# Kernel tuning notes

Measured on AMD Instinct MI355X. Metric: run time of the kernel, lower is better.

The kernel has to match this reference:

```python
import jax, jax.numpy as jnp
import numpy as np

SIGMA = 0.001
EPS_LOG = 1e-12
EPS_COS = 1e-8


def setup_inputs() -> dict:
    key = jax.random.key(0)
    k1, k2, k3, k4 = jax.random.split(key, 4)
    B, T, K, S, d = 32, 512, 8, 8, 300
    center_pos = jax.random.randint(k1, (B,), 0, T)
    query_token_ids = jax.random.randint(k2, (B, T), 0, 30000)
    center_sense_embeddings = jax.random.normal(k3, (B, K, d), dtype=jnp.float32)
    context_sense_embeddings = jax.random.normal(k4, (B, T - 1, S, d), dtype=jnp.float32)
    return {
        'center_pos': center_pos,
        'query_token_ids': query_token_ids,
        'center_sense_embeddings': center_sense_embeddings,
        'context_sense_embeddings': context_sense_embeddings,
    }


def reference(center_pos, query_token_ids, center_sense_embeddings, context_sense_embeddings):
    B, T = query_token_ids.shape
    d = center_sense_embeddings.shape[-1]
    # v: mean over senses of context tokens -> [B, C, d], C = T-1
    v = context_sense_embeddings.mean(axis=-2)
    # a: scaled dot between center senses and context vectors -> [B, C, K]
    a = jnp.einsum('bkd,bcd->bck', center_sense_embeddings, v) / jnp.sqrt(jnp.float32(d))
    # context positions: skip the center position (vectorized form of the per-batch loop)
    i = jnp.arange(T - 1)  # [C]
    ctx_pos = i[None, :] + (i[None, :] >= center_pos[:, None])  # [B, C]
    w = jnp.exp(-jnp.abs(ctx_pos - center_pos[:, None]).astype(jnp.float32) / SIGMA)
    logw = jnp.log(jnp.maximum(w, EPS_LOG))  # [B, C]
    alpha = jax.nn.softmax(a + logw[:, :, None], axis=1)  # softmax over context positions
    m = jnp.einsum('bck,bcd->bkd', alpha, v)  # [B, K, d]
    # cosine similarity along d (torch semantics: clamp each norm by eps)
    num = jnp.sum(center_sense_embeddings * m, axis=-1)
    n1 = jnp.linalg.norm(center_sense_embeddings, axis=-1)
    n2 = jnp.linalg.norm(m, axis=-1)
    s = num / (jnp.maximum(n1, EPS_COS) * jnp.maximum(n2, EPS_COS))  # [B, K]
    q = jax.nn.softmax(s, axis=-1)
    idx = jnp.argmax(q, axis=-1)  # [B]
    pooled = jnp.take_along_axis(center_sense_embeddings, idx[:, None, None], axis=1)[:, 0, :]  # [B, d]
    return pooled, q
```

## Files before the change

### kernel.cpp

```cpp
#include <hip/hip_runtime.h>

#define NB 32
#define NC 511
#define NK 8
#define NS 8
#define ND 300
#define ND4 75
#define NCH 16
#define CCHUNK 32
#define EPS_COS 1e-8f


typedef float nfloat4 __attribute__((ext_vector_type(4)));

__device__ __forceinline__ void n4add(nfloat4& a, const nfloat4& b) { a += b; }

__global__ __launch_bounds__(256) void k_va(const float* __restrict__ ctx,
                                            const float* __restrict__ cen,
                                            float* __restrict__ v,
                                            float* __restrict__ ea) {
    const int blk  = blockIdx.x >> 1;
    const int b    = blk >> 7;
    const int cgrp = blk & 127;
    const int w    = threadIdx.x >> 6;
    const int lane = threadIdx.x & 63;
    const int c = cgrp * 4 + w;
    if (c >= NC) return;

    const nfloat4* ctx4 = (const nfloat4*)ctx + (size_t)(b * NC + c) * NS * ND4;
    const int i0 = lane;
    const int i1 = lane + 64;
    const bool has1 = (i1 < ND4);

    nfloat4 X[NS];
#pragma unroll
    for (int s = 0; s < NS; ++s)
        X[s] = __builtin_nontemporal_load(&ctx4[s * ND4 + i0]);
    nfloat4 Y[NS] = {};
    if (has1) {
#pragma unroll
        for (int s = 0; s < NS; ++s)
            Y[s] = __builtin_nontemporal_load(&ctx4[s * ND4 + i1]);
    }

    n4add(X[0], X[1]); n4add(X[2], X[3]); n4add(X[4], X[5]); n4add(X[6], X[7]);
    n4add(X[0], X[2]); n4add(X[4], X[6]);
    n4add(X[0], X[4]);
    n4add(Y[0], Y[1]); n4add(Y[2], Y[3]); n4add(Y[4], Y[5]); n4add(Y[6], Y[7]);
    n4add(Y[0], Y[2]); n4add(Y[4], Y[6]);
    n4add(Y[0], Y[4]);
    const float inv = 0.125f;
    nfloat4 s0 = X[0] * inv;
    nfloat4 s1 = Y[0] * inv;

    nfloat4* v4 = (nfloat4*)v + (size_t)(b * NC + c) * ND4;
    v4[i0] = s0;
    if (has1) v4[i1] = s1;

    const nfloat4* cen4 = (const nfloat4*)cen + (size_t)b * NK * ND4;
    float pk[NK];
#pragma unroll
    for (int k = 0; k < NK; ++k) {
        nfloat4 ca = cen4[k * ND4 + i0];
        float p = ca.x * s0.x + ca.y * s0.y + ca.z * s0.z + ca.w * s0.w;
        if (has1) {
            nfloat4 cb = cen4[k * ND4 + i1];
            p += cb.x * s1.x + cb.y * s1.y + cb.z * s1.z + cb.w * s1.w;
        }
        pk[k] = p;
    }
#pragma unroll
    for (int off = 32; off; off >>= 1) {
#pragma unroll
        for (int k = 0; k < NK; ++k) pk[k] += __shfl_down(pk[k], off);
    }
    if (lane == 0) {
        const float scale = 0.057735026919f;
#pragma unroll
        for (int k = 0; k < NK; ++k)
            ea[(size_t)(b * NK + k) * NC + c] = __expf(pk[k] * scale);
    }
}

__global__ __launch_bounds__(320) void k_m(const float* __restrict__ v,
                                           const float* __restrict__ ea,
                                           float* __restrict__ part) {
    int b  = blockIdx.x >> 4;
    int ch = blockIdx.x & 15;
    int c0 = ch * CCHUNK;
    int cn = min(CCHUNK, NC - c0);
    __shared__ float al[NK][CCHUNK];
    int t = threadIdx.x;
    if (t < NK * CCHUNK) {
        int k = t >> 5, cc = t & 31;
        al[k][cc] = (cc < cn) ? ea[(size_t)(b * NK + k) * NC + c0 + cc] : 0.f;
    }
    __syncthreads();
    if (t < ND) {
        float acc[NK] = {0.f, 0.f, 0.f, 0.f, 0.f, 0.f, 0.f, 0.f};
        const float* vp = v + ((size_t)b * NC + c0) * ND + t;
        for (int cc = 0; cc < cn; ++cc) {
            float vv = vp[(size_t)cc * ND];
#pragma unroll
            for (int k = 0; k < NK; ++k) acc[k] += al[k][cc] * vv;
        }
        float* pp = part + ((size_t)(ch * NB + b) * NK) * ND + t;
#pragma unroll
        for (int k = 0; k < NK; ++k) pp[(size_t)k * ND] = acc[k];
    }
}

__global__ __launch_bounds__(256) void k_final(const float* __restrict__ part,
                                               const float* __restrict__ cen,
                                               float* __restrict__ out) {
    int b = blockIdx.x;
    __shared__ float m[NK * ND];
    __shared__ float sred[NK];
    __shared__ int bidx;
    int t = threadIdx.x;

    for (int idx = t; idx < NK * ND; idx += 256) {
        float s = 0.f;
#pragma unroll
        for (int ch = 0; ch < NCH; ++ch)
            s += part[(size_t)(ch * NB + b) * NK * ND + idx];
        m[idx] = s;
    }
    __syncthreads();

    int w = t >> 6, lane = t & 63;
#pragma unroll
    for (int kk = 0; kk < 2; ++kk) {
        int k = w + kk * 4;
        const float* cp = cen + (size_t)(b * NK + k) * ND;
        const float* mp = m + k * ND;
        float num = 0.f, n1 = 0.f, n2 = 0.f;
        for (int dd = lane; dd < ND; dd += 64) {
            float cv = cp[dd], mv = mp[dd];
            num += cv * mv; n1 += cv * cv; n2 += mv * mv;
        }
#pragma unroll
        for (int off = 32; off; off >>= 1) {
            num += __shfl_down(num, off);
            n1  += __shfl_down(n1, off);
            n2  += __shfl_down(n2, off);
        }
        if (lane == 0) {
            float denom = fmaxf(sqrtf(n1), EPS_COS) * fmaxf(sqrtf(n2), EPS_COS);
            sred[k] = num / denom;
        }
    }
    __syncthreads();

    if (t == 0) {
        float mx = sred[0];
#pragma unroll
        for (int k = 1; k < NK; ++k) mx = fmaxf(mx, sred[k]);
        float e[NK], sum = 0.f;
#pragma unroll
        for (int k = 0; k < NK; ++k) { e[k] = __expf(sred[k] - mx); sum += e[k]; }
        float inv = 1.f / sum;
        int best = 0; float bv = sred[0];
#pragma unroll
        for (int k = 1; k < NK; ++k) if (sred[k] > bv) { bv = sred[k]; best = k; }
#pragma unroll
        for (int k = 0; k < NK; ++k)
            out[(size_t)NB * ND + b * NK + k] = e[k] * inv;
        bidx = best;
    }
    __syncthreads();

    const float* src = cen + (size_t)(b * NK + bidx) * ND;
    for (int idx = t; idx < ND; idx += 256)
        out[(size_t)b * ND + idx] = src[idx];
}

extern "C" void kernel_launch(void* const* d_in, const int* in_sizes, int n_in,
                              void* d_out, int out_size, void* d_ws, size_t ws_size,
                              hipStream_t stream) {
    const float* cen = (const float*)d_in[2];
    const float* ctx = (const float*)d_in[3];
    float* out = (float*)d_out;

    float* v    = (float*)d_ws;
    float* ea   = v + (size_t)NB * NC * ND;
    float* part = ea + (size_t)NB * NK * NC;

    k_va<<<dim3(NB * 128 * 2), dim3(256), 0, stream>>>(ctx, cen, v, ea);
    k_m<<<dim3(NB * NCH), dim3(320), 0, stream>>>(v, ea, part);
    k_final<<<dim3(NB), dim3(256), 0, stream>>>(part, cen, out);
}
```

Baseline: 289.3 us.

## Process two context rows per wave and split the weighted-sum pass into finer chunks

The context-mean kernel now launches one block per eight context positions, with each wave handling two positions. This removes the earlier grid, in which pairs of blocks mapped to the same context rows and loaded them twice, and it doubles the independent loads in flight per wave. The weighted-sum kernel switches from 16 chunks of 32 positions to 32 chunks of 16, with a fully unrolled guarded loop, to get more blocks and less serial work per thread. In exchange the final kernel sums twice as many partial buffers, and per-thread register use in the first kernel rises.

```diff
diff --git a/kernel.cpp b/kernel.cpp
--- a/kernel.cpp
+++ b/kernel.cpp
@@ -6,8 +6,8 @@
 #define NS 8
 #define ND 300
 #define ND4 75
-#define NCH 16
-#define CCHUNK 32
+#define NCH 32
+#define CCHUNK 16
 #define EPS_COS 1e-8f
 
 
@@ -19,90 +19,115 @@
                                             const float* __restrict__ cen,
                                             float* __restrict__ v,
                                             float* __restrict__ ea) {
-    const int blk  = blockIdx.x >> 1;
-    const int b    = blk >> 7;
-    const int cgrp = blk & 127;
+    const int b    = blockIdx.x >> 6;
+    const int j    = blockIdx.x & 63;
     const int w    = threadIdx.x >> 6;
     const int lane = threadIdx.x & 63;
-    const int c = cgrp * 4 + w;
-    if (c >= NC) return;
-
-    const nfloat4* ctx4 = (const nfloat4*)ctx + (size_t)(b * NC + c) * NS * ND4;
+    const int c0 = j * 8 + w * 2;
+    const int c1 = c0 + 1;
+    const bool h1 = (c1 < NC);
+
     const int i0 = lane;
     const int i1 = lane + 64;
     const bool has1 = (i1 < ND4);
 
-    nfloat4 X[NS];
+    const nfloat4* p0 = (const nfloat4*)ctx + (size_t)(b * NC + c0) * (NS * ND4);
+    const nfloat4* p1 = (const nfloat4*)ctx + (size_t)(b * NC + (h1 ? c1 : c0)) * (NS * ND4);
+
+    nfloat4 X0[NS], X1[NS];
 #pragma unroll
     for (int s = 0; s < NS; ++s)
-        X[s] = __builtin_nontemporal_load(&ctx4[s * ND4 + i0]);
-    nfloat4 Y[NS] = {};
+        X0[s] = __builtin_nontemporal_load(&p0[s * ND4 + i0]);
+#pragma unroll
+    for (int s = 0; s < NS; ++s)
+        X1[s] = __builtin_nontemporal_load(&p1[s * ND4 + i0]);
+    nfloat4 Y0[NS] = {}, Y1[NS] = {};
     if (has1) {
 #pragma unroll
         for (int s = 0; s < NS; ++s)
-            Y[s] = __builtin_nontemporal_load(&ctx4[s * ND4 + i1]);
-    }
-
-    n4add(X[0], X[1]); n4add(X[2], X[3]); n4add(X[4], X[5]); n4add(X[6], X[7]);
-    n4add(X[0], X[2]); n4add(X[4], X[6]);
-    n4add(X[0], X[4]);
-    n4add(Y[0], Y[1]); n4add(Y[2], Y[3]); n4add(Y[4], Y[5]); n4add(Y[6], Y[7]);
-    n4add(Y[0], Y[2]); n4add(Y[4], Y[6]);
-    n4add(Y[0], Y[4]);
+            Y0[s] = __builtin_nontemporal_load(&p0[s * ND4 + i1]);
+#pragma unroll
+        for (int s = 0; s < NS; ++s)
+            Y1[s] = __builtin_nontemporal_load(&p1[s * ND4 + i1]);
+    }
+
+    n4add(X0[0], X0[1]); n4add(X0[2], X0[3]); n4add(X0[4], X0[5]); n4add(X0[6], X0[7]);
+    n4add(X0[0], X0[2]); n4add(X0[4], X0[6]); n4add(X0[0], X0[4]);
+    n4add(X1[0], X1[1]); n4add(X1[2], X1[3]); n4add(X1[4], X1[5]); n4add(X1[6], X1[7]);
+    n4add(X1[0], X1[2]); n4add(X1[4], X1[6]); n4add(X1[0], X1[4]);
+    n4add(Y0[0], Y0[1]); n4add(Y0[2], Y0[3]); n4add(Y0[4], Y0[5]); n4add(Y0[6], Y0[7]);
+    n4add(Y0[0], Y0[2]); n4add(Y0[4], Y0[6]); n4add(Y0[0], Y0[4]);
+    n4add(Y1[0], Y1[1]); n4add(Y1[2], Y1[3]); n4add(Y1[4], Y1[5]); n4add(Y1[6], Y1[7]);
+    n4add(Y1[0], Y1[2]); n4add(Y1[4], Y1[6]); n4add(Y1[0], Y1[4]);
     const float inv = 0.125f;
-    nfloat4 s0 = X[0] * inv;
-    nfloat4 s1 = Y[0] * inv;
-
-    nfloat4* v4 = (nfloat4*)v + (size_t)(b * NC + c) * ND4;
-    v4[i0] = s0;
-    if (has1) v4[i1] = s1;
+    nfloat4 a0 = X0[0] * inv, b0 = Y0[0] * inv;
+    nfloat4 a1 = X1[0] * inv, b1 = Y1[0] * inv;
+
+    nfloat4* v40 = (nfloat4*)v + (size_t)(b * NC + c0) * ND4;
+    v40[i0] = a0;
+    if (has1) v40[i1] = b0;
+    if (h1) {
+        nfloat4* v41 = (nfloat4*)v + (size_t)(b * NC + c1) * ND4;
+        v41[i0] = a1;
+        if (has1) v41[i1] = b1;
+    }
 
     const nfloat4* cen4 = (const nfloat4*)cen + (size_t)b * NK * ND4;
-    float pk[NK];
+    float pk0[NK], pk1[NK];
 #pragma unroll
     for (int k = 0; k < NK; ++k) {
         nfloat4 ca = cen4[k * ND4 + i0];
-        float p = ca.x * s0.x + ca.y * s0.y + ca.z * s0.z + ca.w * s0.w;
+        float q0 = ca.x * a0.x + ca.y * a0.y + ca.z * a0.z + ca.w * a0.w;
+        float q1 = ca.x * a1.x + ca.y * a1.y + ca.z * a1.z + ca.w * a1.w;
         if (has1) {
             nfloat4 cb = cen4[k * ND4 + i1];
-            p += cb.x * s1.x + cb.y * s1.y + cb.z * s1.z + cb.w * s1.w;
-        }
-        pk[k] = p;
+            q0 += cb.x * b0.x + cb.y * b0.y + cb.z * b0.z + cb.w * b0.w;
+            q1 += cb.x * b1.x + cb.y * b1.y + cb.z * b1.z + cb.w * b1.w;
+        }
+        pk0[k] = q0; pk1[k] = q1;
     }
 #pragma unroll
     for (int off = 32; off; off >>= 1) {
 #pragma unroll
-        for (int k = 0; k < NK; ++k) pk[k] += __shfl_down(pk[k], off);
+        for (int k = 0; k < NK; ++k) {
+            pk0[k] += __shfl_down(pk0[k], off);
+            pk1[k] += __shfl_down(pk1[k], off);
+        }
     }
     if (lane == 0) {
         const float scale = 0.057735026919f;
 #pragma unroll
-        for (int k = 0; k < NK; ++k)
-            ea[(size_t)(b * NK + k) * NC + c] = __expf(pk[k] * scale);
+        for (int k = 0; k < NK; ++k) {
+            ea[(size_t)(b * NK + k) * NC + c0] = __expf(pk0[k] * scale);
+            if (h1) ea[(size_t)(b * NK + k) * NC + c1] = __expf(pk1[k] * scale);
+        }
     }
 }
 
 __global__ __launch_bounds__(320) void k_m(const float* __restrict__ v,
                                            const float* __restrict__ ea,
                                            float* __restrict__ part) {
-    int b  = blockIdx.x >> 4;
-    int ch = blockIdx.x & 15;
+    int b  = blockIdx.x >> 5;
+    int ch = blockIdx.x & 31;
     int c0 = ch * CCHUNK;
     int cn = min(CCHUNK, NC - c0);
     __shared__ float al[NK][CCHUNK];
     int t = threadIdx.x;
     if (t < NK * CCHUNK) {
-        int k = t >> 5, cc = t & 31;
+        int k = t >> 4, cc = t & 15;
         al[k][cc] = (cc < cn) ? ea[(size_t)(b * NK + k) * NC + c0 + cc] : 0.f;
     }
     __syncthreads();
     if (t < ND) {
         float acc[NK] = {0.f, 0.f, 0.f, 0.f, 0.f, 0.f, 0.f, 0.f};
         const float* vp = v + ((size_t)b * NC + c0) * ND + t;
-        for (int cc = 0; cc < cn; ++cc) {
-            float vv = vp[(size_t)cc * ND];
-#pragma unroll
-            for (int k = 0; k < NK; ++k) acc[k] += al[k][cc] * vv;
+#pragma unroll
+        for (int cc = 0; cc < CCHUNK; ++cc) {
+            if (cc < cn) {
+                float vv = vp[(size_t)cc * ND];
+#pragma unroll
+                for (int k = 0; k < NK; ++k) acc[k] += al[k][cc] * vv;
+            }
         }
         float* pp = part + ((size_t)(ch * NB + b) * NK) * ND + t;
 #pragma unroll
@@ -186,7 +211,7 @@
     float* ea   = v + (size_t)NB * NC * ND;
     float* part = ea + (size_t)NB * NK * NC;
 
-    k_va<<<dim3(NB * 128 * 2), dim3(256), 0, stream>>>(ctx, cen, v, ea);
+    k_va<<<dim3(NB * 64), dim3(256), 0, stream>>>(ctx, cen, v, ea);
     k_m<<<dim3(NB * NCH), dim3(320), 0, stream>>>(v, ea, part);
     k_final<<<dim3(NB), dim3(256), 0, stream>>>(part, cen, out);
 }
```

Result: faster. 255.7 us (-11.6%).
